# Performance work log

Hardware: AMD Instinct MI355X
Metric: run time of the kernel (lower is better)

The kernel has to match this reference:

```python
import jax, jax.numpy as jnp
import numpy as np

EMBED_DIM = 1024
NUM_HEADS = 16
HEAD_DIM = EMBED_DIM // NUM_HEADS
B, N = 4, 2048
EPS = 1e-5


def rotate_half(x):
    x2d = x.reshape(x.shape[:-1] + (-1, 2))
    x1, x2 = x2d[..., 0], x2d[..., 1]
    return jnp.stack([-x2, x1], axis=-1).reshape(x.shape)


def apply_rotary_emb(freqs, t):
    return t * freqs[0] + rotate_half(t) * freqs[1]


def setup_inputs() -> dict:
    key = jax.random.key(0)
    ks = jax.random.split(key, 12)
    d = EMBED_DIM
    inp = {
        "x": jax.random.normal(ks[0], (B, N, d), jnp.float32),
        "encoding": jax.random.normal(ks[1], (2, N, HEAD_DIM), jnp.float32),
        "Wqkv_w": jax.random.normal(ks[2], (d, 3 * d), jnp.float32) * (1.0 / np.sqrt(d)),
        "Wqkv_b": jnp.zeros((3 * d,), jnp.float32),
        "out_w": jax.random.normal(ks[3], (d, d), jnp.float32) * (1.0 / np.sqrt(d)),
        "out_b": jnp.zeros((d,), jnp.float32),
        "ffn0_w": jax.random.normal(ks[4], (2 * d, 2 * d), jnp.float32) * (1.0 / np.sqrt(2 * d)),
        "ffn0_b": jnp.zeros((2 * d,), jnp.float32),
        "ln_scale": jnp.ones((2 * d,), jnp.float32),
        "ln_bias": jnp.zeros((2 * d,), jnp.float32),
        "ffn3_w": jax.random.normal(ks[5], (2 * d, d), jnp.float32) * (1.0 / np.sqrt(2 * d)),
        "ffn3_b": jnp.zeros((d,), jnp.float32),
    }
    return inp


def reference(x, encoding, Wqkv_w, Wqkv_b, out_w, out_b, ffn0_w, ffn0_b, ln_scale, ln_bias, ffn3_w, ffn3_b):
    b, n, d = x.shape
    # fused QKV projection
    qkv = jnp.einsum('bnd,de->bne', x, Wqkv_w) + Wqkv_b
    qkv = qkv.reshape(b, n, NUM_HEADS, HEAD_DIM, 3).transpose(0, 2, 1, 3, 4)  # (b,h,n,hd,3)
    q, k, v = qkv[..., 0], qkv[..., 1], qkv[..., 2]
    # RoPE (encoding broadcasts over batch/heads)
    q = apply_rotary_emb(encoding, q)
    k = apply_rotary_emb(encoding, k)
    # attention (no mask)
    scale = 1.0 / jnp.sqrt(jnp.asarray(HEAD_DIM, x.dtype))
    logits = jnp.einsum('bhqd,bhkd->bhqk', q, k) * scale
    attn = jax.nn.softmax(logits, axis=-1)
    context = jnp.einsum('bhqk,bhkd->bhqd', attn, v)
    message = context.transpose(0, 2, 1, 3).reshape(b, n, d)
    message = jnp.einsum('bnd,de->bne', message, out_w) + out_b
    # FFN: concat -> Dense -> LayerNorm -> GELU(exact) -> Dense
    h = jnp.concatenate([x, message], axis=-1)
    h = jnp.einsum('bnd,de->bne', h, ffn0_w) + ffn0_b
    mu = jnp.mean(h, axis=-1, keepdims=True)
    var = jnp.mean(jnp.square(h - mu), axis=-1, keepdims=True)
    h = (h - mu) * jax.lax.rsqrt(var + EPS) * ln_scale + ln_bias
    h = jax.nn.gelu(h, approximate=False)
    res = jnp.einsum('bnd,de->bne', h, ffn3_w) + ffn3_b
    return x + res
```

## Files before the change

kernel.cpp:

```cpp
#include <hip/hip_runtime.h>
#include <hip/hip_bf16.h>
#include <math.h>

typedef __bf16 bf16x8 __attribute__((ext_vector_type(8)));
typedef float f32x4 __attribute__((ext_vector_type(4)));

#define MFMA16(a, b, c) __builtin_amdgcn_mfma_f32_16x16x32_bf16((a), (b), (c), 0, 0, 0)

__device__ __forceinline__ void gload16(const void* g, void* l) {
  __builtin_amdgcn_global_load_lds((const __attribute__((address_space(1))) void*)g,
                                   (__attribute__((address_space(3))) void*)l, 16, 0, 0);
}

#define BARRIER asm volatile("s_barrier" ::: "memory")

__device__ __forceinline__ void tr_body(float (*tile)[33], const float* __restrict__ in,
                                        int ldin, __bf16* __restrict__ out, int ldo,
                                        int n0, int k0, int t) {
  int tx = t & 31, ty = t >> 5;
#pragma unroll
  for (int r = 0; r < 32; r += 8)
    tile[ty + r][tx] = in[(size_t)(k0 + ty + r) * ldin + n0 + tx];
  __syncthreads();
#pragma unroll
  for (int r = 0; r < 32; r += 8)
    out[(size_t)(n0 + ty + r) * ldo + k0 + tx] = (__bf16)tile[tx][ty + r];
}

__global__ __launch_bounds__(256) void prep1(
    const float* __restrict__ wqkv, __bf16* __restrict__ wT_qkv,
    const float* __restrict__ wffn0, __bf16* __restrict__ wT_ffn0,
    __bf16* __restrict__ w0bT,
    const float* __restrict__ wffn3, __bf16* __restrict__ wT_ffn3,
    const float* __restrict__ wout, __bf16* __restrict__ wout_bf,
    const float* __restrict__ bqkv, float* __restrict__ bqkv_p,
    const float* __restrict__ bout, float* __restrict__ bias_part,
    const float* __restrict__ x, __bf16* __restrict__ h_in) {
  __shared__ float tile[32][33];
  const int bid = blockIdx.x;
  const int t = threadIdx.x;

  if (bid < 3072) {
    int bx = bid % 96, by = bid / 96;
    int n0 = bx * 32, k0 = by * 32;
    int tx = t & 31, ty = t >> 5;
#pragma unroll
    for (int r = 0; r < 32; r += 8)
      tile[ty + r][tx] = wqkv[(size_t)(k0 + ty + r) * 3072 + n0 + tx];
    __syncthreads();
#pragma unroll
    for (int r = 0; r < 32; r += 8) {
      int n = n0 + ty + r;
      int h = n / 192, rem = n % 192, hd = rem / 3, which = rem % 3;
      int np = which * 1024 + h * 64 + hd;
      wT_qkv[(size_t)np * 1024 + k0 + tx] = (__bf16)tile[tx][ty + r];
    }
  } else if (bid < 5120) {
    int lb = bid - 3072, bx = lb % 64, by = lb / 64;
    tr_body(tile, wffn0, 2048, wT_ffn0, 2048, bx * 32, by * 32, t);
  } else if (bid < 7168) {
    int lb = bid - 5120, bx = lb % 64, by = lb / 64;
    tr_body(tile, wffn0 + (size_t)1024 * 2048, 2048, w0bT, 1024, bx * 32, by * 32, t);
  } else if (bid < 9216) {
    int lb = bid - 7168, bx = lb % 32, by = lb / 32;
    tr_body(tile, wffn3, 1024, wT_ffn3, 2048, bx * 32, by * 32, t);
  } else if (bid < 9728) {
    int id = (bid - 9216) * 256 + t;
    const float* src = wout + (size_t)id * 8;
    __bf16 tmp[8];
#pragma unroll
    for (int e = 0; e < 8; ++e) tmp[e] = (__bf16)src[e];
    *(uint4*)(wout_bf + (size_t)id * 8) = *(uint4*)tmp;
  } else if (bid < 9740) {
    int n = (bid - 9728) * 256 + t;
    if (n < 3072) {
      int h = n / 192, rem = n % 192, hd = rem / 3, which = rem % 3;
      bqkv_p[which * 1024 + h * 64 + hd] = bqkv[n];
    }
  } else if (bid < 9868) {
    int lb = bid - 9740;
    int n = (lb % 8) * 256 + t;
    int e0 = (lb / 8) * 64;
    float s = 0.f;
#pragma unroll 4
    for (int e = 0; e < 64; ++e)
      s += bout[e0 + e] * wffn0[(size_t)(1024 + e0 + e) * 2048 + n];
    bias_part[(size_t)(lb / 8) * 2048 + n] = s;
  } else {
    int id = (bid - 9868) * 256 + t;
    int row = id >> 7, cc = id & 127;
    const float* src = x + (size_t)row * 1024 + cc * 8;
    __bf16 tmp[8];
#pragma unroll
    for (int e = 0; e < 8; ++e) tmp[e] = (__bf16)src[e];
    *(uint4*)(h_in + (size_t)row * 2048 + cc * 8) = *(uint4*)tmp;
  }
}

__global__ __launch_bounds__(256) void prep2(
    const __bf16* __restrict__ w0bT, const __bf16* __restrict__ wout_bf,
    __bf16* __restrict__ wT_ffn0,
    const float* __restrict__ bias_part, const float* __restrict__ bffn0,
    float* __restrict__ bffn0_f) {
  const int bid = blockIdx.x;
  const int t = threadIdx.x;
  if (bid >= 128) {
    int n = (bid - 128) * 256 + t;
    float s = bffn0[n];
#pragma unroll
    for (int y = 0; y < 16; ++y) s += bias_part[(size_t)y * 2048 + n];
    bffn0_f[n] = s;
    return;
  }
  __shared__ __attribute__((aligned(16))) __bf16 As[128 * 64];
  __shared__ __attribute__((aligned(16))) __bf16 Bs[128 * 64];
  const int row0A = (bid % 16) * 128;
  const int row0B = (bid / 16) * 128;
  const int wave = t >> 6, lane = t & 63;
  const int wm = wave >> 1, wn = wave & 1;
  const int g = lane >> 4, lr = lane & 15;
  f32x4 acc[4][4] = {};
  for (int k0 = 0; k0 < 1024; k0 += 64) {
#pragma unroll
    for (int p = 0; p < 4; ++p) {
      int cbase = (wave * 4 + p) * 64;
      int ci = cbase + lane;
      int r = ci >> 3, cp = ci & 7, cl = cp ^ (r & 7);
      gload16(w0bT + (size_t)(row0A + r) * 1024 + k0 + cl * 8, &As[cbase * 8]);
      gload16(wout_bf + (size_t)(row0B + r) * 1024 + k0 + cl * 8, &Bs[cbase * 8]);
    }
    __syncthreads();
#pragma unroll
    for (int kk = 0; kk < 2; ++kk) {
      bf16x8 af[4], bfr[4];
#pragma unroll
      for (int mt = 0; mt < 4; ++mt) {
        int r = wm * 64 + mt * 16 + lr, c = kk * 4 + g;
        af[mt] = *(const bf16x8*)((char*)As + r * 128 + ((c ^ (r & 7)) * 16));
      }
#pragma unroll
      for (int nt = 0; nt < 4; ++nt) {
        int r = wn * 64 + nt * 16 + lr, c = kk * 4 + g;
        bfr[nt] = *(const bf16x8*)((char*)Bs + r * 128 + ((c ^ (r & 7)) * 16));
      }
#pragma unroll
      for (int mt = 0; mt < 4; ++mt)
#pragma unroll
        for (int nt = 0; nt < 4; ++nt)
          acc[mt][nt] = MFMA16(af[mt], bfr[nt], acc[mt][nt]);
    }
    __syncthreads();
  }
#pragma unroll
  for (int mt = 0; mt < 4; ++mt) {
    int grow_base = row0A + wm * 64 + mt * 16 + g * 4;
#pragma unroll
    for (int nt = 0; nt < 4; ++nt) {
      int gcol = row0B + wn * 64 + nt * 16 + lr;
#pragma unroll
      for (int j = 0; j < 4; ++j)
        wT_ffn0[(size_t)(grow_base + j) * 2048 + 1024 + gcol] = (__bf16)acc[mt][nt][j];
    }
  }
}

template <typename OutT, bool HAS_RES, bool HAS_BIAS>
__global__ __launch_bounds__(256) void gemm_kernel(
    const __bf16* __restrict__ A, int lda,
    const __bf16* __restrict__ Bt,
    const float* __restrict__ bias,
    OutT* __restrict__ C, int ldc,
    const float* __restrict__ res,
    int M, int Nn, int K) {
  __shared__ __attribute__((aligned(16))) __bf16 As[128 * 64];
  __shared__ __attribute__((aligned(16))) __bf16 Bs[128 * 64];

  const int t = threadIdx.x;
  const int row0A = blockIdx.x * 128;
  const int row0B = blockIdx.y * 128;
  const int wave = t >> 6, lane = t & 63;
  const int wm = wave >> 1, wn = wave & 1;
  const int g = lane >> 4, lr = lane & 15;

  f32x4 acc[4][4] = {};

  for (int k0 = 0; k0 < K; k0 += 64) {
#pragma unroll
    for (int p = 0; p < 4; ++p) {
      int cbase = (wave * 4 + p) * 64;
      int ci = cbase + lane;
      int r = ci >> 3, cp = ci & 7, cl = cp ^ (r & 7);
      gload16(A + (size_t)(row0A + r) * lda + k0 + cl * 8, &As[cbase * 8]);
      gload16(Bt + (size_t)(row0B + r) * K + k0 + cl * 8, &Bs[cbase * 8]);
    }
    __syncthreads();
#pragma unroll
    for (int kk = 0; kk < 2; ++kk) {
      bf16x8 af[4], bfr[4];
#pragma unroll
      for (int mt = 0; mt < 4; ++mt) {
        int r = wm * 64 + mt * 16 + lr, c = kk * 4 + g;
        af[mt] = *(const bf16x8*)((char*)As + r * 128 + ((c ^ (r & 7)) * 16));
      }
#pragma unroll
      for (int nt = 0; nt < 4; ++nt) {
        int r = wn * 64 + nt * 16 + lr, c = kk * 4 + g;
        bfr[nt] = *(const bf16x8*)((char*)Bs + r * 128 + ((c ^ (r & 7)) * 16));
      }
#pragma unroll
      for (int mt = 0; mt < 4; ++mt)
#pragma unroll
        for (int nt = 0; nt < 4; ++nt)
          acc[mt][nt] = MFMA16(af[mt], bfr[nt], acc[mt][nt]);
    }
    __syncthreads();
  }

  float bias_v[4];
#pragma unroll
  for (int nt = 0; nt < 4; ++nt)
    bias_v[nt] = HAS_BIAS ? bias[row0B + wn * 64 + nt * 16 + lr] : 0.f;
#pragma unroll
  for (int mt = 0; mt < 4; ++mt) {
    int grow_base = row0A + wm * 64 + mt * 16 + g * 4;
#pragma unroll
    for (int nt = 0; nt < 4; ++nt) {
      int gcol = row0B + wn * 64 + nt * 16 + lr;
#pragma unroll
      for (int j = 0; j < 4; ++j) {
        int grow = grow_base + j;
        float v = acc[mt][nt][j] + bias_v[nt];
        if (HAS_RES) v += res[(size_t)grow * ldc + gcol];
        C[(size_t)grow * ldc + gcol] = (OutT)v;
      }
    }
  }
}

template <typename OutT>
__global__ __launch_bounds__(512, 2) void gemm256p(
    const __bf16* __restrict__ A, int lda,
    const __bf16* __restrict__ Bt, int ldb,
    const float* __restrict__ bias,
    OutT* __restrict__ C, int ldc, int K) {
  __shared__ __attribute__((aligned(16))) __bf16 As[2][256 * 64];
  __shared__ __attribute__((aligned(16))) __bf16 Bs[2][256 * 64];

  const int t = threadIdx.x;
  const int wave = t >> 6, lane = t & 63;
  const int wm = wave >> 2, wn = wave & 3;
  const int g = lane >> 4, lr = lane & 15;
  const int row0A = blockIdx.x * 256, row0B = blockIdx.y * 256;
  const int L = K >> 6;

  f32x4 acc[8][4] = {};

#define STG_A(tile, i)                                                        \
  {                                                                           \
    int cb = ((i) * 8 + wave) * 64;                                           \
    int ci = cb + lane;                                                       \
    int r = ci >> 3, cl = (ci & 7) ^ (r & 7);                                 \
    gload16(A + (size_t)(row0A + r) * lda + (size_t)(tile) * 64 + cl * 8,     \
            &As[(tile) & 1][cb * 8]);                                         \
  }
#define STG_B(tile, i)                                                        \
  {                                                                           \
    int cb = ((i) * 8 + wave) * 64;                                           \
    int ci = cb + lane;                                                       \
    int r = ci >> 3, cl = (ci & 7) ^ (r & 7);                                 \
    gload16(Bt + (size_t)(row0B + r) * ldb + (size_t)(tile) * 64 + cl * 8,    \
            &Bs[(tile) & 1][cb * 8]);                                         \
  }
#define AFRAG(d, mi, ks)                                                      \
  (*(const bf16x8*)((const char*)As[d] + (wm * 128 + (mi) * 16 + lr) * 128 +  \
                    ((((ks) * 4 + g) ^ (lr & 7)) * 16)))
#define BFRAG(d, ni, ks)                                                      \
  (*(const bf16x8*)((const char*)Bs[d] + (wn * 64 + (ni) * 16 + lr) * 128 +   \
                    ((((ks) * 4 + g) ^ (lr & 7)) * 16)))

#pragma unroll
  for (int i = 0; i < 4; ++i) STG_A(0, i);
#pragma unroll
  for (int i = 0; i < 4; ++i) STG_B(0, i);
  STG_A(1, 0);
  STG_A(1, 1);
  asm volatile("s_waitcnt vmcnt(2)" ::: "memory");
  BARRIER;

  for (int tt = 0; tt < L; ++tt) {
    const int d = tt & 1;
    const bool s1 = (tt + 1) < L, s2 = (tt + 2) < L;
    bf16x8 aL[4][2], aH[4][2], bL[2][2], bH[2][2];

#pragma unroll
    for (int mi = 0; mi < 4; ++mi) {
      aL[mi][0] = AFRAG(d, mi, 0);
      aL[mi][1] = AFRAG(d, mi, 1);
    }
#pragma unroll
    for (int ni = 0; ni < 2; ++ni) {
      bL[ni][0] = BFRAG(d, ni, 0);
      bL[ni][1] = BFRAG(d, ni, 1);
    }
    if (s1) { STG_A(tt + 1, 2); STG_A(tt + 1, 3); }
    BARRIER;
    __builtin_amdgcn_s_setprio(1);
#pragma unroll
    for (int mi = 0; mi < 4; ++mi)
#pragma unroll
      for (int ni = 0; ni < 2; ++ni) {
        acc[mi][ni] = MFMA16(aL[mi][0], bL[ni][0], acc[mi][ni]);
        acc[mi][ni] = MFMA16(aL[mi][1], bL[ni][1], acc[mi][ni]);
      }
    __builtin_amdgcn_s_setprio(0);
    BARRIER;

#pragma unroll
    for (int ni = 0; ni < 2; ++ni) {
      bH[ni][0] = BFRAG(d, ni + 2, 0);
      bH[ni][1] = BFRAG(d, ni + 2, 1);
    }
    if (s1) { STG_B(tt + 1, 0); STG_B(tt + 1, 1); }
    BARRIER;
    __builtin_amdgcn_s_setprio(1);
#pragma unroll
    for (int mi = 0; mi < 4; ++mi)
#pragma unroll
      for (int ni = 0; ni < 2; ++ni) {
        acc[mi][ni + 2] = MFMA16(aL[mi][0], bH[ni][0], acc[mi][ni + 2]);
        acc[mi][ni + 2] = MFMA16(aL[mi][1], bH[ni][1], acc[mi][ni + 2]);
      }
    __builtin_amdgcn_s_setprio(0);
    BARRIER;

#pragma unroll
    for (int mi = 0; mi < 4; ++mi) {
      aH[mi][0] = AFRAG(d, mi + 4, 0);
      aH[mi][1] = AFRAG(d, mi + 4, 1);
    }
    if (s1) { STG_B(tt + 1, 2); STG_B(tt + 1, 3); }
    BARRIER;
    __builtin_amdgcn_s_setprio(1);
#pragma unroll
    for (int mi = 0; mi < 4; ++mi)
#pragma unroll
      for (int ni = 0; ni < 2; ++ni) {
        acc[mi + 4][ni + 2] = MFMA16(aH[mi][0], bH[ni][0], acc[mi + 4][ni + 2]);
        acc[mi + 4][ni + 2] = MFMA16(aH[mi][1], bH[ni][1], acc[mi + 4][ni + 2]);
      }
    __builtin_amdgcn_s_setprio(0);
    BARRIER;

    if (s2) { STG_A(tt + 2, 0); STG_A(tt + 2, 1); }
    __builtin_amdgcn_s_setprio(1);
#pragma unroll
    for (int mi = 0; mi < 4; ++mi)
#pragma unroll
      for (int ni = 0; ni < 2; ++ni) {
        acc[mi + 4][ni] = MFMA16(aH[mi][0], bL[ni][0], acc[mi + 4][ni]);
        acc[mi + 4][ni] = MFMA16(aH[mi][1], bL[ni][1], acc[mi + 4][ni]);
      }
    __builtin_amdgcn_s_setprio(0);
    if (s2)
      asm volatile("s_waitcnt vmcnt(2)" ::: "memory");
    else
      asm volatile("s_waitcnt vmcnt(0)" ::: "memory");
    BARRIER;
  }
#undef STG_A
#undef STG_B
#undef AFRAG
#undef BFRAG

  float bias_v[4];
#pragma unroll
  for (int ni = 0; ni < 4; ++ni) bias_v[ni] = bias[row0B + wn * 64 + ni * 16 + lr];
#pragma unroll
  for (int mi = 0; mi < 8; ++mi) {
    int grow_base = row0A + wm * 128 + mi * 16 + g * 4;
#pragma unroll
    for (int ni = 0; ni < 4; ++ni) {
      int gcol = row0B + wn * 64 + ni * 16 + lr;
#pragma unroll
      for (int j = 0; j < 4; ++j)
        C[(size_t)(grow_base + j) * ldc + gcol] = (OutT)(acc[mi][ni][j] + bias_v[ni]);
    }
  }
}

__global__ __launch_bounds__(256) void rope_scatter(
    const __bf16* __restrict__ qkv, const float* __restrict__ enc,
    __bf16* __restrict__ q, __bf16* __restrict__ kk, __bf16* __restrict__ vt) {
  int bh = blockIdx.y;
  int b = bh >> 4, h = bh & 15;
  int n0 = blockIdx.x * 64;
  int t = threadIdx.x;
  const float QSC = 0.125f * 1.44269504088896f;
#pragma unroll
  for (int i = 0; i < 2; ++i) {
    int id = t + i * 256;
    int nl = id >> 3, cc = id & 7;
    int n = n0 + nl;
    size_t row = (size_t)(b * 2048 + n) * 3072;
    bf16x8 qv = *(const bf16x8*)(qkv + row + h * 64 + cc * 8);
    bf16x8 kv = *(const bf16x8*)(qkv + row + 1024 + h * 64 + cc * 8);
    const float* e0 = enc + (size_t)n * 64 + cc * 8;
    const float* e1 = e0 + 131072;
    __bf16 qo[8], ko[8];
#pragma unroll
    for (int e = 0; e < 8; e += 2) {
      float q0 = (float)qv[e], q1 = (float)qv[e + 1];
      float k0 = (float)kv[e], k1 = (float)kv[e + 1];
      float f00 = e0[e], f01 = e0[e + 1], f10 = e1[e], f11 = e1[e + 1];
      qo[e] = (__bf16)((q0 * f00 - q1 * f10) * QSC);
      qo[e + 1] = (__bf16)((q1 * f01 + q0 * f11) * QSC);
      ko[e] = (__bf16)(k0 * f00 - k1 * f10);
      ko[e + 1] = (__bf16)(k1 * f01 + k0 * f11);
    }
    size_t qb = ((size_t)bh * 2048 + n) * 64 + cc * 8;
    *(uint4*)(q + qb) = *(uint4*)qo;
    *(uint4*)(kk + qb) = *(uint4*)ko;
  }
#pragma unroll
  for (int i = 0; i < 2; ++i) {
    int id = t + i * 256;
    int hd = id >> 3, c = id & 7;
    __bf16 tmp[8];
#pragma unroll
    for (int e = 0; e < 8; ++e) {
      int kv = (c >> 2) * 32 + (e >> 2) * 16 + (c & 3) * 4 + (e & 3);
      int n = n0 + kv;
      tmp[e] = qkv[(size_t)(b * 2048 + n) * 3072 + 2048 + h * 64 + hd];
    }
    *(uint4*)(vt + ((size_t)bh * 64 + hd) * 2048 + n0 + c * 8) = *(uint4*)tmp;
  }
}

__global__ __launch_bounds__(256) void attn_kernel(
    const __bf16* __restrict__ q, const __bf16* __restrict__ k,
    const __bf16* __restrict__ vt, __bf16* __restrict__ ctx) {
  __shared__ __attribute__((aligned(16))) __bf16 Ks[2][64 * 64];
  __shared__ __attribute__((aligned(16))) __bf16 Vs[2][64 * 64];

  int bid0 = blockIdx.y * gridDim.x + blockIdx.x;
  int bid = (bid0 & 7) * 64 + (bid0 >> 3);
  const int bh = bid >> 3, qblk = bid & 7;
  const int b = bh >> 4, h = bh & 15;
  const int q0 = qblk * 256;
  const int t = threadIdx.x, wave = t >> 6, lane = t & 63;
  const int g = lane >> 4, lr = lane & 15;
  const int qrow0 = q0 + wave * 64;

  const __bf16* kbase = k + (size_t)bh * 2048 * 64;
  const __bf16* vbase = vt + (size_t)bh * 64 * 2048;

  bf16x8 qf[4][2];
#pragma unroll
  for (int u = 0; u < 4; ++u)
#pragma unroll
    for (int kc = 0; kc < 2; ++kc)
      qf[u][kc] = *(const bf16x8*)(q + ((size_t)bh * 2048 + qrow0 + u * 16 + lr) * 64 +
                                   kc * 32 + g * 8);

  bf16x8 ones;
#pragma unroll
  for (int e = 0; e < 8; ++e) ones[e] = (__bf16)1.0f;

  f32x4 o[4][4] = {};
  f32x4 lacc[4] = {};

#define STAGE_ATTN(buf, kv0)                                                    \
  {                                                                             \
    _Pragma("unroll") for (int p = 0; p < 2; ++p) {                             \
      int cbase = wave * 128 + p * 64;                                          \
      int ci = cbase + lane;                                                    \
      int r = ci >> 3, cp = ci & 7, cl = cp ^ (r & 7);                          \
      gload16(kbase + (size_t)((kv0) + r) * 64 + cl * 8, &Ks[buf][cbase * 8]);  \
      gload16(vbase + (size_t)r * 2048 + (kv0) + cl * 8, &Vs[buf][cbase * 8]);  \
    }                                                                           \
  }

  STAGE_ATTN(0, 0);
  __syncthreads();
  int buf = 0;

  for (int kv0 = 0; kv0 < 2048; kv0 += 64) {
    if (kv0 + 64 < 2048) STAGE_ATTN(buf ^ 1, kv0 + 64);

    bf16x8 kf[4][2];
#pragma unroll
    for (int nt = 0; nt < 4; ++nt) {
      int r = nt * 16 + lr;
      kf[nt][0] = *(const bf16x8*)((char*)Ks[buf] + r * 128 + ((g ^ (r & 7)) * 16));
      kf[nt][1] = *(const bf16x8*)((char*)Ks[buf] + r * 128 + (((4 + g) ^ (r & 7)) * 16));
    }

    bf16x8 pf[4][2];
#pragma unroll
    for (int u = 0; u < 4; ++u) {
      f32x4 s[4];
      __builtin_amdgcn_s_setprio(1);
#pragma unroll
      for (int nt = 0; nt < 4; ++nt) {
        f32x4 a = {};
        a = MFMA16(kf[nt][0], qf[u][0], a);
        a = MFMA16(kf[nt][1], qf[u][1], a);
        s[nt] = a;
      }
      __builtin_amdgcn_s_setprio(0);
#pragma unroll
      for (int t2 = 0; t2 < 2; ++t2)
#pragma unroll
        for (int e = 0; e < 8; ++e)
          pf[u][t2][e] = (__bf16)__builtin_amdgcn_exp2f(s[2 * t2 + (e >> 2)][e & 3]);
    }

    __builtin_amdgcn_s_setprio(1);
#pragma unroll
    for (int u = 0; u < 4; ++u) {
      lacc[u] = MFMA16(ones, pf[u][0], lacc[u]);
      lacc[u] = MFMA16(ones, pf[u][1], lacc[u]);
    }
#pragma unroll
    for (int t2 = 0; t2 < 2; ++t2)
#pragma unroll
      for (int nt = 0; nt < 4; ++nt) {
        int r = nt * 16 + lr;
        bf16x8 vf = *(const bf16x8*)((char*)Vs[buf] + r * 128 + (((t2 * 4 + g) ^ (r & 7)) * 16));
#pragma unroll
        for (int u = 0; u < 4; ++u) o[u][nt] = MFMA16(vf, pf[u][t2], o[u][nt]);
      }
    __builtin_amdgcn_s_setprio(0);
    __syncthreads();
    buf ^= 1;
  }

#pragma unroll
  for (int u = 0; u < 4; ++u) {
    float inv = 1.f / lacc[u][0];
    size_t obase = ((size_t)(b * 2048 + qrow0 + u * 16 + lr)) * 2048 + 1024 + h * 64;
#pragma unroll
    for (int nt = 0; nt < 4; ++nt) {
      __bf16 w4[4];
#pragma unroll
      for (int j = 0; j < 4; ++j) w4[j] = (__bf16)(o[u][nt][j] * inv);
      *(uint2*)(ctx + obase + nt * 16 + g * 4) = *(uint2*)w4;
    }
  }
#undef STAGE_ATTN
}

__global__ __launch_bounds__(256) void ln_gelu(const __bf16* __restrict__ hin,
                                               const float* __restrict__ lns,
                                               const float* __restrict__ lnb,
                                               __bf16* __restrict__ hout) {
  int row = blockIdx.x;
  const __bf16* rp = hin + (size_t)row * 2048;
  int t = threadIdx.x;
  __bf16 tmp[8];
  *(uint4*)tmp = *(const uint4*)(rp + t * 8);
  float vals[8], s = 0.f, s2 = 0.f;
#pragma unroll
  for (int e = 0; e < 8; ++e) {
    float x = (float)tmp[e];
    vals[e] = x;
    s += x;
    s2 += x * x;
  }
#pragma unroll
  for (int m = 1; m < 64; m <<= 1) {
    s += __shfl_xor(s, m, 64);
    s2 += __shfl_xor(s2, m, 64);
  }
  __shared__ float red[8];
  int wave = t >> 6, lane = t & 63;
  if (lane == 0) { red[wave] = s; red[4 + wave] = s2; }
  __syncthreads();
  s = red[0] + red[1] + red[2] + red[3];
  s2 = red[4] + red[5] + red[6] + red[7];
  float mu = s * (1.f / 2048.f);
  float var = s2 * (1.f / 2048.f) - mu * mu;
  float rstd = rsqrtf(var + 1e-5f);
  __bf16 outv[8];
#pragma unroll
  for (int e = 0; e < 8; ++e) {
    int c = t * 8 + e;
    float xh = (vals[e] - mu) * rstd * lns[c] + lnb[c];
    float gg = 0.5f * xh * (1.f + erff(xh * 0.70710678118f));
    outv[e] = (__bf16)gg;
  }
  *(uint4*)(hout + (size_t)row * 2048 + t * 8) = *(uint4*)outv;
}

extern "C" void kernel_launch(void* const* d_in, const int* in_sizes, int n_in,
                              void* d_out, int out_size, void* d_ws, size_t ws_size,
                              hipStream_t stream) {
  const float* x = (const float*)d_in[0];
  const float* enc = (const float*)d_in[1];
  const float* wqkv = (const float*)d_in[2];
  const float* bqkv = (const float*)d_in[3];
  const float* wout = (const float*)d_in[4];
  const float* bout = (const float*)d_in[5];
  const float* wffn0 = (const float*)d_in[6];
  const float* bffn0 = (const float*)d_in[7];
  const float* lns = (const float*)d_in[8];
  const float* lnb = (const float*)d_in[9];
  const float* wffn3 = (const float*)d_in[10];
  const float* bffn3 = (const float*)d_in[11];
  float* out = (float*)d_out;
  char* ws = (char*)d_ws;

  __bf16* wT_qkv = (__bf16*)(ws + 0);
  __bf16* wT_ffn0 = (__bf16*)(ws + 6291456);
  __bf16* wT_ffn3 = (__bf16*)(ws + 14680064);
  __bf16* wout_bf = (__bf16*)(ws + 18874368);
  __bf16* w0bT = (__bf16*)(ws + 20971520);
  float* bias_part = (float*)(ws + 25165824);
  float* bqkv_p = (float*)(ws + 25296896);
  float* bffn0_f = (float*)(ws + 25309184);
  __bf16* h_in = (__bf16*)(ws + 25317376);
  __bf16* qkv = (__bf16*)(ws + 58871808);
  __bf16* ffn0o = qkv;
  __bf16* qb = (__bf16*)(ws + 109203456);
  __bf16* h2 = qb;
  __bf16* kb = (__bf16*)(ws + 125980672);
  __bf16* vtb = (__bf16*)(ws + 142757888);

  dim3 blk(256);
  prep1<<<13964, blk, 0, stream>>>(wqkv, wT_qkv, wffn0, wT_ffn0, w0bT, wffn3, wT_ffn3,
                                   wout, wout_bf, bqkv, bqkv_p, bout, bias_part, x, h_in);
  prep2<<<136, blk, 0, stream>>>(w0bT, wout_bf, wT_ffn0, bias_part, bffn0, bffn0_f);

  gemm256p<__bf16><<<dim3(32, 12), dim3(512), 0, stream>>>(
      h_in, 2048, wT_qkv, 1024, bqkv_p, qkv, 3072, 1024);

  rope_scatter<<<dim3(32, 64), blk, 0, stream>>>(qkv, enc, qb, kb, vtb);
  attn_kernel<<<dim3(8, 64), blk, 0, stream>>>(qb, kb, vtb, h_in);

  gemm256p<__bf16><<<dim3(32, 8), dim3(512), 0, stream>>>(
      h_in, 2048, wT_ffn0, 2048, bffn0_f, ffn0o, 2048, 2048);

  ln_gelu<<<8192, blk, 0, stream>>>(ffn0o, lns, lnb, h2);

  gemm_kernel<float, true, true><<<dim3(64, 8), blk, 0, stream>>>(
      h2, 2048, wT_ffn3, bffn3, out, 1024, x, 8192, 1024, 2048);
}
```

Measured before the change: 372.5 us.

## Fuse RoPE and Q/K/V scatter into QKV GEMM epilogue; halve attention query tile

The QKV GEMM epilogue now applies RoPE and scaling and writes Q, K and transposed V straight into their per-head layouts. This removes the separate rope_scatter kernel and the round trip of the full qkv intermediate through memory. A transposed copy of the encoding table is made in prep1 so the epilogue can read it with float4 loads, and V is transposed through LDS. Separately, attention now handles 128 query rows per block instead of 256, doubling the grid for better occupancy and cutting register pressure, at the cost of reloading K/V tiles more often.

```diff
diff --git a/kernel.cpp b/kernel.cpp
--- a/kernel.cpp
+++ b/kernel.cpp
@@ -35,7 +35,8 @@
     const float* __restrict__ wout, __bf16* __restrict__ wout_bf,
     const float* __restrict__ bqkv, float* __restrict__ bqkv_p,
     const float* __restrict__ bout, float* __restrict__ bias_part,
-    const float* __restrict__ x, __bf16* __restrict__ h_in) {
+    const float* __restrict__ x, __bf16* __restrict__ h_in,
+    const float* __restrict__ enc, float* __restrict__ encT) {
   __shared__ float tile[32][33];
   const int bid = blockIdx.x;
   const int t = threadIdx.x;
@@ -86,7 +87,7 @@
     for (int e = 0; e < 64; ++e)
       s += bout[e0 + e] * wffn0[(size_t)(1024 + e0 + e) * 2048 + n];
     bias_part[(size_t)(lb / 8) * 2048 + n] = s;
-  } else {
+  } else if (bid < 13964) {
     int id = (bid - 9868) * 256 + t;
     int row = id >> 7, cc = id & 127;
     const float* src = x + (size_t)row * 1024 + cc * 8;
@@ -94,6 +95,19 @@
 #pragma unroll
     for (int e = 0; e < 8; ++e) tmp[e] = (__bf16)src[e];
     *(uint4*)(h_in + (size_t)row * 2048 + cc * 8) = *(uint4*)tmp;
+  } else {
+    int lb = bid - 13964;
+    int tab = lb >> 7, lb2 = lb & 127;
+    int n0 = (lb2 & 1) * 32;
+    int k0 = (lb2 >> 1) * 32;
+    int tx = t & 31, ty = t >> 5;
+#pragma unroll
+    for (int r = 0; r < 32; r += 8)
+      tile[ty + r][tx] = enc[(size_t)tab * 131072 + (size_t)(k0 + ty + r) * 64 + n0 + tx];
+    __syncthreads();
+#pragma unroll
+    for (int r = 0; r < 32; r += 8)
+      encT[(size_t)tab * 131072 + (size_t)(n0 + ty + r) * 2048 + k0 + tx] = tile[tx][ty + r];
   }
 }
 
@@ -237,12 +251,14 @@
   }
 }
 
-template <typename OutT>
+template <typename OutT, int MODE>
 __global__ __launch_bounds__(512, 2) void gemm256p(
     const __bf16* __restrict__ A, int lda,
     const __bf16* __restrict__ Bt, int ldb,
     const float* __restrict__ bias,
-    OutT* __restrict__ C, int ldc, int K) {
+    OutT* __restrict__ C, int ldc, int K,
+    __bf16* __restrict__ qb, __bf16* __restrict__ kb,
+    __bf16* __restrict__ vtb, const float* __restrict__ encT) {
   __shared__ __attribute__((aligned(16))) __bf16 As[2][256 * 64];
   __shared__ __attribute__((aligned(16))) __bf16 Bs[2][256 * 64];
 
@@ -375,64 +391,78 @@
   float bias_v[4];
 #pragma unroll
   for (int ni = 0; ni < 4; ++ni) bias_v[ni] = bias[row0B + wn * 64 + ni * 16 + lr];
-#pragma unroll
-  for (int mi = 0; mi < 8; ++mi) {
-    int grow_base = row0A + wm * 128 + mi * 16 + g * 4;
-#pragma unroll
-    for (int ni = 0; ni < 4; ++ni) {
-      int gcol = row0B + wn * 64 + ni * 16 + lr;
-#pragma unroll
-      for (int j = 0; j < 4; ++j)
-        C[(size_t)(grow_base + j) * ldc + gcol] = (OutT)(acc[mi][ni][j] + bias_v[ni]);
-    }
-  }
-}
-
-__global__ __launch_bounds__(256) void rope_scatter(
-    const __bf16* __restrict__ qkv, const float* __restrict__ enc,
-    __bf16* __restrict__ q, __bf16* __restrict__ kk, __bf16* __restrict__ vt) {
-  int bh = blockIdx.y;
-  int b = bh >> 4, h = bh & 15;
-  int n0 = blockIdx.x * 64;
-  int t = threadIdx.x;
-  const float QSC = 0.125f * 1.44269504088896f;
-#pragma unroll
-  for (int i = 0; i < 2; ++i) {
-    int id = t + i * 256;
-    int nl = id >> 3, cc = id & 7;
-    int n = n0 + nl;
-    size_t row = (size_t)(b * 2048 + n) * 3072;
-    bf16x8 qv = *(const bf16x8*)(qkv + row + h * 64 + cc * 8);
-    bf16x8 kv = *(const bf16x8*)(qkv + row + 1024 + h * 64 + cc * 8);
-    const float* e0 = enc + (size_t)n * 64 + cc * 8;
-    const float* e1 = e0 + 131072;
-    __bf16 qo[8], ko[8];
-#pragma unroll
-    for (int e = 0; e < 8; e += 2) {
-      float q0 = (float)qv[e], q1 = (float)qv[e + 1];
-      float k0 = (float)kv[e], k1 = (float)kv[e + 1];
-      float f00 = e0[e], f01 = e0[e + 1], f10 = e1[e], f11 = e1[e + 1];
-      qo[e] = (__bf16)((q0 * f00 - q1 * f10) * QSC);
-      qo[e + 1] = (__bf16)((q1 * f01 + q0 * f11) * QSC);
-      ko[e] = (__bf16)(k0 * f00 - k1 * f10);
-      ko[e + 1] = (__bf16)(k1 * f01 + k0 * f11);
-    }
-    size_t qb = ((size_t)bh * 2048 + n) * 64 + cc * 8;
-    *(uint4*)(q + qb) = *(uint4*)qo;
-    *(uint4*)(kk + qb) = *(uint4*)ko;
-  }
-#pragma unroll
-  for (int i = 0; i < 2; ++i) {
-    int id = t + i * 256;
-    int hd = id >> 3, c = id & 7;
-    __bf16 tmp[8];
-#pragma unroll
-    for (int e = 0; e < 8; ++e) {
-      int kv = (c >> 2) * 32 + (e >> 2) * 16 + (c & 3) * 4 + (e & 3);
-      int n = n0 + kv;
-      tmp[e] = qkv[(size_t)(b * 2048 + n) * 3072 + 2048 + h * 64 + hd];
-    }
-    *(uint4*)(vt + ((size_t)bh * 64 + hd) * 2048 + n0 + c * 8) = *(uint4*)tmp;
+
+  if (MODE == 0) {
+#pragma unroll
+    for (int mi = 0; mi < 8; ++mi) {
+      int grow_base = row0A + wm * 128 + mi * 16 + g * 4;
+#pragma unroll
+      for (int ni = 0; ni < 4; ++ni) {
+        int gcol = row0B + wn * 64 + ni * 16 + lr;
+#pragma unroll
+        for (int j = 0; j < 4; ++j)
+          C[(size_t)(grow_base + j) * ldc + gcol] = (OutT)(acc[mi][ni][j] + bias_v[ni]);
+      }
+    }
+  } else {
+    const int which = blockIdx.y >> 2;
+    const int h = (blockIdx.y & 3) * 4 + wn;
+    const int b = blockIdx.x >> 3;
+    const int bh = b * 16 + h;
+    const int ntop = (blockIdx.x & 7) * 256 + wm * 128;
+
+    if (which < 2) {
+      __bf16* dst = (which == 0) ? qb : kb;
+      const float sc = (which == 0) ? 0.125f * 1.44269504088896f : 1.f;
+      const float sgn = (lane & 1) ? 1.f : -1.f;
+#pragma unroll
+      for (int mi = 0; mi < 8; ++mi) {
+#pragma unroll
+        for (int ni = 0; ni < 4; ++ni) {
+          int hd = ni * 16 + lr;
+          const float* p0 = encT + (size_t)hd * 2048 + ntop + mi * 16 + g * 4;
+          float4 f0 = *(const float4*)p0;
+          float4 f1 = *(const float4*)(p0 + 131072);
+#pragma unroll
+          for (int j = 0; j < 4; ++j) {
+            float v = acc[mi][ni][j] + bias_v[ni];
+            float p = __shfl_xor(v, 1, 64);
+            float e0 = ((const float*)&f0)[j], e1 = ((const float*)&f1)[j];
+            float r = (v * e0 + sgn * p * e1) * sc;
+            dst[((size_t)bh * 2048 + ntop + mi * 16 + g * 4 + j) * 64 + hd] = (__bf16)r;
+          }
+        }
+      }
+    } else {
+      char* lbuf = (char*)As;
+      const int wb2 = wave * 16384;
+#pragma unroll
+      for (int mi = 0; mi < 8; ++mi)
+#pragma unroll
+        for (int ni = 0; ni < 4; ++ni) {
+          int hd = ni * 16 + lr;
+          int tok = mi * 16 + g * 4;
+          __bf16 w4[4];
+#pragma unroll
+          for (int j = 0; j < 4; ++j) w4[j] = (__bf16)(acc[mi][ni][j] + bias_v[ni]);
+          int ab = wb2 + hd * 256 + ((tok * 2) ^ ((hd & 15) << 4));
+          *(uint2*)(lbuf + ab) = *(uint2*)w4;
+        }
+      __syncthreads();
+#pragma unroll
+      for (int it = 0; it < 16; ++it) {
+        int hd = (lane >> 3) + (it & 7) * 8;
+        int slot = (lane & 7) + (it >> 3) * 8;
+        int grp = slot >> 3, c = slot & 7;
+        int kv0 = grp * 64 + (c >> 2) * 32 + (c & 3) * 4;
+        int a1 = wb2 + hd * 256 + ((kv0 * 2) ^ ((hd & 15) << 4));
+        int a2 = wb2 + hd * 256 + (((kv0 + 16) * 2) ^ ((hd & 15) << 4));
+        uint2 lo = *(uint2*)(lbuf + a1);
+        uint2 hi = *(uint2*)(lbuf + a2);
+        uint4 o4 = make_uint4(lo.x, lo.y, hi.x, hi.y);
+        *(uint4*)(vtb + ((size_t)bh * 64 + hd) * 2048 + ntop + grp * 64 + c * 8) = o4;
+      }
+    }
   }
 }
 
@@ -442,21 +472,22 @@
   __shared__ __attribute__((aligned(16))) __bf16 Ks[2][64 * 64];
   __shared__ __attribute__((aligned(16))) __bf16 Vs[2][64 * 64];
 
+  int nwg = gridDim.x * gridDim.y;
   int bid0 = blockIdx.y * gridDim.x + blockIdx.x;
-  int bid = (bid0 & 7) * 64 + (bid0 >> 3);
-  const int bh = bid >> 3, qblk = bid & 7;
+  int bid = (bid0 & 7) * (nwg >> 3) + (bid0 >> 3);
+  const int bh = bid >> 4, qblk = bid & 15;
   const int b = bh >> 4, h = bh & 15;
-  const int q0 = qblk * 256;
+  const int q0 = qblk * 128;
   const int t = threadIdx.x, wave = t >> 6, lane = t & 63;
   const int g = lane >> 4, lr = lane & 15;
-  const int qrow0 = q0 + wave * 64;
+  const int qrow0 = q0 + wave * 32;
 
   const __bf16* kbase = k + (size_t)bh * 2048 * 64;
   const __bf16* vbase = vt + (size_t)bh * 64 * 2048;
 
-  bf16x8 qf[4][2];
-#pragma unroll
-  for (int u = 0; u < 4; ++u)
+  bf16x8 qf[2][2];
+#pragma unroll
+  for (int u = 0; u < 2; ++u)
 #pragma unroll
     for (int kc = 0; kc < 2; ++kc)
       qf[u][kc] = *(const bf16x8*)(q + ((size_t)bh * 2048 + qrow0 + u * 16 + lr) * 64 +
@@ -466,8 +497,8 @@
 #pragma unroll
   for (int e = 0; e < 8; ++e) ones[e] = (__bf16)1.0f;
 
-  f32x4 o[4][4] = {};
-  f32x4 lacc[4] = {};
+  f32x4 o[2][4] = {};
+  f32x4 lacc[2] = {};
 
 #define STAGE_ATTN(buf, kv0)                                                    \
   {                                                                             \
@@ -487,56 +518,49 @@
   for (int kv0 = 0; kv0 < 2048; kv0 += 64) {
     if (kv0 + 64 < 2048) STAGE_ATTN(buf ^ 1, kv0 + 64);
 
-    bf16x8 kf[4][2];
+    f32x4 s[2][4];
+    __builtin_amdgcn_s_setprio(1);
 #pragma unroll
     for (int nt = 0; nt < 4; ++nt) {
       int r = nt * 16 + lr;
-      kf[nt][0] = *(const bf16x8*)((char*)Ks[buf] + r * 128 + ((g ^ (r & 7)) * 16));
-      kf[nt][1] = *(const bf16x8*)((char*)Ks[buf] + r * 128 + (((4 + g) ^ (r & 7)) * 16));
-    }
-
-    bf16x8 pf[4][2];
-#pragma unroll
-    for (int u = 0; u < 4; ++u) {
-      f32x4 s[4];
+      bf16x8 kf0 = *(const bf16x8*)((char*)Ks[buf] + r * 128 + ((g ^ (r & 7)) * 16));
+      bf16x8 kf1 = *(const bf16x8*)((char*)Ks[buf] + r * 128 + (((4 + g) ^ (r & 7)) * 16));
+#pragma unroll
+      for (int u = 0; u < 2; ++u) {
+        f32x4 a = {};
+        a = MFMA16(kf0, qf[u][0], a);
+        a = MFMA16(kf1, qf[u][1], a);
+        s[u][nt] = a;
+      }
+    }
+    __builtin_amdgcn_s_setprio(0);
+
+#pragma unroll
+    for (int t2 = 0; t2 < 2; ++t2) {
+      bf16x8 pf[2];
+#pragma unroll
+      for (int u = 0; u < 2; ++u) {
+#pragma unroll
+        for (int e = 0; e < 8; ++e)
+          pf[u][e] = (__bf16)__builtin_amdgcn_exp2f(s[u][2 * t2 + (e >> 2)][e & 3]);
+        lacc[u] = MFMA16(ones, pf[u], lacc[u]);
+      }
       __builtin_amdgcn_s_setprio(1);
-#pragma unroll
-      for (int nt = 0; nt < 4; ++nt) {
-        f32x4 a = {};
-        a = MFMA16(kf[nt][0], qf[u][0], a);
-        a = MFMA16(kf[nt][1], qf[u][1], a);
-        s[nt] = a;
-      }
-      __builtin_amdgcn_s_setprio(0);
-#pragma unroll
-      for (int t2 = 0; t2 < 2; ++t2)
-#pragma unroll
-        for (int e = 0; e < 8; ++e)
-          pf[u][t2][e] = (__bf16)__builtin_amdgcn_exp2f(s[2 * t2 + (e >> 2)][e & 3]);
-    }
-
-    __builtin_amdgcn_s_setprio(1);
-#pragma unroll
-    for (int u = 0; u < 4; ++u) {
-      lacc[u] = MFMA16(ones, pf[u][0], lacc[u]);
-      lacc[u] = MFMA16(ones, pf[u][1], lacc[u]);
-    }
-#pragma unroll
-    for (int t2 = 0; t2 < 2; ++t2)
 #pragma unroll
       for (int nt = 0; nt < 4; ++nt) {
         int r = nt * 16 + lr;
         bf16x8 vf = *(const bf16x8*)((char*)Vs[buf] + r * 128 + (((t2 * 4 + g) ^ (r & 7)) * 16));
 #pragma unroll
-        for (int u = 0; u < 4; ++u) o[u][nt] = MFMA16(vf, pf[u][t2], o[u][nt]);
-      }
-    __builtin_amdgcn_s_setprio(0);
+        for (int u = 0; u < 2; ++u) o[u][nt] = MFMA16(vf, pf[u], o[u][nt]);
+      }
+      __builtin_amdgcn_s_setprio(0);
+    }
     __syncthreads();
     buf ^= 1;
   }
 
 #pragma unroll
-  for (int u = 0; u < 4; ++u) {
+  for (int u = 0; u < 2; ++u) {
     float inv = 1.f / lacc[u][0];
     size_t obase = ((size_t)(b * 2048 + qrow0 + u * 16 + lr)) * 2048 + 1024 + h * 64;
 #pragma unroll
@@ -619,26 +643,27 @@
   float* bqkv_p = (float*)(ws + 25296896);
   float* bffn0_f = (float*)(ws + 25309184);
   __bf16* h_in = (__bf16*)(ws + 25317376);
-  __bf16* qkv = (__bf16*)(ws + 58871808);
-  __bf16* ffn0o = qkv;
+  __bf16* ffn0o = (__bf16*)(ws + 58871808);
   __bf16* qb = (__bf16*)(ws + 109203456);
   __bf16* h2 = qb;
   __bf16* kb = (__bf16*)(ws + 125980672);
   __bf16* vtb = (__bf16*)(ws + 142757888);
+  float* encT = (float*)(ws + 159535104);
 
   dim3 blk(256);
-  prep1<<<13964, blk, 0, stream>>>(wqkv, wT_qkv, wffn0, wT_ffn0, w0bT, wffn3, wT_ffn3,
-                                   wout, wout_bf, bqkv, bqkv_p, bout, bias_part, x, h_in);
+  prep1<<<14220, blk, 0, stream>>>(wqkv, wT_qkv, wffn0, wT_ffn0, w0bT, wffn3, wT_ffn3,
+                                   wout, wout_bf, bqkv, bqkv_p, bout, bias_part, x, h_in,
+                                   enc, encT);
   prep2<<<136, blk, 0, stream>>>(w0bT, wout_bf, wT_ffn0, bias_part, bffn0, bffn0_f);
 
-  gemm256p<__bf16><<<dim3(32, 12), dim3(512), 0, stream>>>(
-      h_in, 2048, wT_qkv, 1024, bqkv_p, qkv, 3072, 1024);
-
-  rope_scatter<<<dim3(32, 64), blk, 0, stream>>>(qkv, enc, qb, kb, vtb);
-  attn_kernel<<<dim3(8, 64), blk, 0, stream>>>(qb, kb, vtb, h_in);
-
-  gemm256p<__bf16><<<dim3(32, 8), dim3(512), 0, stream>>>(
-      h_in, 2048, wT_ffn0, 2048, bffn0_f, ffn0o, 2048, 2048);
+  gemm256p<__bf16, 1><<<dim3(32, 12), dim3(512), 0, stream>>>(
+      h_in, 2048, wT_qkv, 1024, bqkv_p, (__bf16*)nullptr, 0, 1024, qb, kb, vtb, encT);
+
+  attn_kernel<<<dim3(16, 64), blk, 0, stream>>>(qb, kb, vtb, h_in);
+
+  gemm256p<__bf16, 0><<<dim3(32, 8), dim3(512), 0, stream>>>(
+      h_in, 2048, wT_ffn0, 2048, bffn0_f, ffn0o, 2048, 2048,
+      nullptr, nullptr, nullptr, nullptr);
 
   ln_gelu<<<8192, blk, 0, stream>>>(ffn0o, lns, lnb, h2);
 
```

New measurement: 365.0 us. -2.0%, faster.

## Replace 256-tile GEMMs with generic GEMM and halve attention query tile

Applied to the files above, without the earlier changes.

Removes the 256x256 ping-pong GEMM kernel and routes the QKV and FFN0 projections through the existing 128-tile gemm_kernel with larger grids. The attention kernel now handles 128 query rows per block (32 per wave), doubling the grid to 1024 blocks. It also interleaves exp, row-sum and PV MFMAs per half-tile to cut register pressure. This trades per-tile data reuse for more parallelism and occupancy, but risks losing the efficiency of the tuned large-tile GEMM.

```diff
diff --git a/kernel.cpp b/kernel.cpp
--- a/kernel.cpp
+++ b/kernel.cpp
@@ -11,8 +11,6 @@
   __builtin_amdgcn_global_load_lds((const __attribute__((address_space(1))) void*)g,
                                    (__attribute__((address_space(3))) void*)l, 16, 0, 0);
 }
-
-#define BARRIER asm volatile("s_barrier" ::: "memory")
 
 __device__ __forceinline__ void tr_body(float (*tile)[33], const float* __restrict__ in,
                                         int ldin, __bf16* __restrict__ out, int ldo,
@@ -237,157 +235,6 @@
   }
 }
 
-template <typename OutT>
-__global__ __launch_bounds__(512, 2) void gemm256p(
-    const __bf16* __restrict__ A, int lda,
-    const __bf16* __restrict__ Bt, int ldb,
-    const float* __restrict__ bias,
-    OutT* __restrict__ C, int ldc, int K) {
-  __shared__ __attribute__((aligned(16))) __bf16 As[2][256 * 64];
-  __shared__ __attribute__((aligned(16))) __bf16 Bs[2][256 * 64];
-
-  const int t = threadIdx.x;
-  const int wave = t >> 6, lane = t & 63;
-  const int wm = wave >> 2, wn = wave & 3;
-  const int g = lane >> 4, lr = lane & 15;
-  const int row0A = blockIdx.x * 256, row0B = blockIdx.y * 256;
-  const int L = K >> 6;
-
-  f32x4 acc[8][4] = {};
-
-#define STG_A(tile, i)                                                        \
-  {                                                                           \
-    int cb = ((i) * 8 + wave) * 64;                                           \
-    int ci = cb + lane;                                                       \
-    int r = ci >> 3, cl = (ci & 7) ^ (r & 7);                                 \
-    gload16(A + (size_t)(row0A + r) * lda + (size_t)(tile) * 64 + cl * 8,     \
-            &As[(tile) & 1][cb * 8]);                                         \
-  }
-#define STG_B(tile, i)                                                        \
-  {                                                                           \
-    int cb = ((i) * 8 + wave) * 64;                                           \
-    int ci = cb + lane;                                                       \
-    int r = ci >> 3, cl = (ci & 7) ^ (r & 7);                                 \
-    gload16(Bt + (size_t)(row0B + r) * ldb + (size_t)(tile) * 64 + cl * 8,    \
-            &Bs[(tile) & 1][cb * 8]);                                         \
-  }
-#define AFRAG(d, mi, ks)                                                      \
-  (*(const bf16x8*)((const char*)As[d] + (wm * 128 + (mi) * 16 + lr) * 128 +  \
-                    ((((ks) * 4 + g) ^ (lr & 7)) * 16)))
-#define BFRAG(d, ni, ks)                                                      \
-  (*(const bf16x8*)((const char*)Bs[d] + (wn * 64 + (ni) * 16 + lr) * 128 +   \
-                    ((((ks) * 4 + g) ^ (lr & 7)) * 16)))
-
-#pragma unroll
-  for (int i = 0; i < 4; ++i) STG_A(0, i);
-#pragma unroll
-  for (int i = 0; i < 4; ++i) STG_B(0, i);
-  STG_A(1, 0);
-  STG_A(1, 1);
-  asm volatile("s_waitcnt vmcnt(2)" ::: "memory");
-  BARRIER;
-
-  for (int tt = 0; tt < L; ++tt) {
-    const int d = tt & 1;
-    const bool s1 = (tt + 1) < L, s2 = (tt + 2) < L;
-    bf16x8 aL[4][2], aH[4][2], bL[2][2], bH[2][2];
-
-#pragma unroll
-    for (int mi = 0; mi < 4; ++mi) {
-      aL[mi][0] = AFRAG(d, mi, 0);
-      aL[mi][1] = AFRAG(d, mi, 1);
-    }
-#pragma unroll
-    for (int ni = 0; ni < 2; ++ni) {
-      bL[ni][0] = BFRAG(d, ni, 0);
-      bL[ni][1] = BFRAG(d, ni, 1);
-    }
-    if (s1) { STG_A(tt + 1, 2); STG_A(tt + 1, 3); }
-    BARRIER;
-    __builtin_amdgcn_s_setprio(1);
-#pragma unroll
-    for (int mi = 0; mi < 4; ++mi)
-#pragma unroll
-      for (int ni = 0; ni < 2; ++ni) {
-        acc[mi][ni] = MFMA16(aL[mi][0], bL[ni][0], acc[mi][ni]);
-        acc[mi][ni] = MFMA16(aL[mi][1], bL[ni][1], acc[mi][ni]);
-      }
-    __builtin_amdgcn_s_setprio(0);
-    BARRIER;
-
-#pragma unroll
-    for (int ni = 0; ni < 2; ++ni) {
-      bH[ni][0] = BFRAG(d, ni + 2, 0);
-      bH[ni][1] = BFRAG(d, ni + 2, 1);
-    }
-    if (s1) { STG_B(tt + 1, 0); STG_B(tt + 1, 1); }
-    BARRIER;
-    __builtin_amdgcn_s_setprio(1);
-#pragma unroll
-    for (int mi = 0; mi < 4; ++mi)
-#pragma unroll
-      for (int ni = 0; ni < 2; ++ni) {
-        acc[mi][ni + 2] = MFMA16(aL[mi][0], bH[ni][0], acc[mi][ni + 2]);
-        acc[mi][ni + 2] = MFMA16(aL[mi][1], bH[ni][1], acc[mi][ni + 2]);
-      }
-    __builtin_amdgcn_s_setprio(0);
-    BARRIER;
-
-#pragma unroll
-    for (int mi = 0; mi < 4; ++mi) {
-      aH[mi][0] = AFRAG(d, mi + 4, 0);
-      aH[mi][1] = AFRAG(d, mi + 4, 1);
-    }
-    if (s1) { STG_B(tt + 1, 2); STG_B(tt + 1, 3); }
-    BARRIER;
-    __builtin_amdgcn_s_setprio(1);
-#pragma unroll
-    for (int mi = 0; mi < 4; ++mi)
-#pragma unroll
-      for (int ni = 0; ni < 2; ++ni) {
-        acc[mi + 4][ni + 2] = MFMA16(aH[mi][0], bH[ni][0], acc[mi + 4][ni + 2]);
-        acc[mi + 4][ni + 2] = MFMA16(aH[mi][1], bH[ni][1], acc[mi + 4][ni + 2]);
-      }
-    __builtin_amdgcn_s_setprio(0);
-    BARRIER;
-
-    if (s2) { STG_A(tt + 2, 0); STG_A(tt + 2, 1); }
-    __builtin_amdgcn_s_setprio(1);
-#pragma unroll
-    for (int mi = 0; mi < 4; ++mi)
-#pragma unroll
-      for (int ni = 0; ni < 2; ++ni) {
-        acc[mi + 4][ni] = MFMA16(aH[mi][0], bL[ni][0], acc[mi + 4][ni]);
-        acc[mi + 4][ni] = MFMA16(aH[mi][1], bL[ni][1], acc[mi + 4][ni]);
-      }
-    __builtin_amdgcn_s_setprio(0);
-    if (s2)
-      asm volatile("s_waitcnt vmcnt(2)" ::: "memory");
-    else
-      asm volatile("s_waitcnt vmcnt(0)" ::: "memory");
-    BARRIER;
-  }
-#undef STG_A
-#undef STG_B
-#undef AFRAG
-#undef BFRAG
-
-  float bias_v[4];
-#pragma unroll
-  for (int ni = 0; ni < 4; ++ni) bias_v[ni] = bias[row0B + wn * 64 + ni * 16 + lr];
-#pragma unroll
-  for (int mi = 0; mi < 8; ++mi) {
-    int grow_base = row0A + wm * 128 + mi * 16 + g * 4;
-#pragma unroll
-    for (int ni = 0; ni < 4; ++ni) {
-      int gcol = row0B + wn * 64 + ni * 16 + lr;
-#pragma unroll
-      for (int j = 0; j < 4; ++j)
-        C[(size_t)(grow_base + j) * ldc + gcol] = (OutT)(acc[mi][ni][j] + bias_v[ni]);
-    }
-  }
-}
-
 __global__ __launch_bounds__(256) void rope_scatter(
     const __bf16* __restrict__ qkv, const float* __restrict__ enc,
     __bf16* __restrict__ q, __bf16* __restrict__ kk, __bf16* __restrict__ vt) {
@@ -442,21 +289,22 @@
   __shared__ __attribute__((aligned(16))) __bf16 Ks[2][64 * 64];
   __shared__ __attribute__((aligned(16))) __bf16 Vs[2][64 * 64];
 
+  int nwg = gridDim.x * gridDim.y;
   int bid0 = blockIdx.y * gridDim.x + blockIdx.x;
-  int bid = (bid0 & 7) * 64 + (bid0 >> 3);
-  const int bh = bid >> 3, qblk = bid & 7;
+  int bid = (bid0 & 7) * (nwg >> 3) + (bid0 >> 3);
+  const int bh = bid >> 4, qblk = bid & 15;
   const int b = bh >> 4, h = bh & 15;
-  const int q0 = qblk * 256;
+  const int q0 = qblk * 128;
   const int t = threadIdx.x, wave = t >> 6, lane = t & 63;
   const int g = lane >> 4, lr = lane & 15;
-  const int qrow0 = q0 + wave * 64;
+  const int qrow0 = q0 + wave * 32;
 
   const __bf16* kbase = k + (size_t)bh * 2048 * 64;
   const __bf16* vbase = vt + (size_t)bh * 64 * 2048;
 
-  bf16x8 qf[4][2];
-#pragma unroll
-  for (int u = 0; u < 4; ++u)
+  bf16x8 qf[2][2];
+#pragma unroll
+  for (int u = 0; u < 2; ++u)
 #pragma unroll
     for (int kc = 0; kc < 2; ++kc)
       qf[u][kc] = *(const bf16x8*)(q + ((size_t)bh * 2048 + qrow0 + u * 16 + lr) * 64 +
@@ -466,8 +314,8 @@
 #pragma unroll
   for (int e = 0; e < 8; ++e) ones[e] = (__bf16)1.0f;
 
-  f32x4 o[4][4] = {};
-  f32x4 lacc[4] = {};
+  f32x4 o[2][4] = {};
+  f32x4 lacc[2] = {};
 
 #define STAGE_ATTN(buf, kv0)                                                    \
   {                                                                             \
@@ -487,56 +335,49 @@
   for (int kv0 = 0; kv0 < 2048; kv0 += 64) {
     if (kv0 + 64 < 2048) STAGE_ATTN(buf ^ 1, kv0 + 64);
 
-    bf16x8 kf[4][2];
+    f32x4 s[2][4];
+    __builtin_amdgcn_s_setprio(1);
 #pragma unroll
     for (int nt = 0; nt < 4; ++nt) {
       int r = nt * 16 + lr;
-      kf[nt][0] = *(const bf16x8*)((char*)Ks[buf] + r * 128 + ((g ^ (r & 7)) * 16));
-      kf[nt][1] = *(const bf16x8*)((char*)Ks[buf] + r * 128 + (((4 + g) ^ (r & 7)) * 16));
-    }
-
-    bf16x8 pf[4][2];
-#pragma unroll
-    for (int u = 0; u < 4; ++u) {
-      f32x4 s[4];
+      bf16x8 kf0 = *(const bf16x8*)((char*)Ks[buf] + r * 128 + ((g ^ (r & 7)) * 16));
+      bf16x8 kf1 = *(const bf16x8*)((char*)Ks[buf] + r * 128 + (((4 + g) ^ (r & 7)) * 16));
+#pragma unroll
+      for (int u = 0; u < 2; ++u) {
+        f32x4 a = {};
+        a = MFMA16(kf0, qf[u][0], a);
+        a = MFMA16(kf1, qf[u][1], a);
+        s[u][nt] = a;
+      }
+    }
+    __builtin_amdgcn_s_setprio(0);
+
+#pragma unroll
+    for (int t2 = 0; t2 < 2; ++t2) {
+      bf16x8 pf[2];
+#pragma unroll
+      for (int u = 0; u < 2; ++u) {
+#pragma unroll
+        for (int e = 0; e < 8; ++e)
+          pf[u][e] = (__bf16)__builtin_amdgcn_exp2f(s[u][2 * t2 + (e >> 2)][e & 3]);
+        lacc[u] = MFMA16(ones, pf[u], lacc[u]);
+      }
       __builtin_amdgcn_s_setprio(1);
-#pragma unroll
-      for (int nt = 0; nt < 4; ++nt) {
-        f32x4 a = {};
-        a = MFMA16(kf[nt][0], qf[u][0], a);
-        a = MFMA16(kf[nt][1], qf[u][1], a);
-        s[nt] = a;
-      }
-      __builtin_amdgcn_s_setprio(0);
-#pragma unroll
-      for (int t2 = 0; t2 < 2; ++t2)
-#pragma unroll
-        for (int e = 0; e < 8; ++e)
-          pf[u][t2][e] = (__bf16)__builtin_amdgcn_exp2f(s[2 * t2 + (e >> 2)][e & 3]);
-    }
-
-    __builtin_amdgcn_s_setprio(1);
-#pragma unroll
-    for (int u = 0; u < 4; ++u) {
-      lacc[u] = MFMA16(ones, pf[u][0], lacc[u]);
-      lacc[u] = MFMA16(ones, pf[u][1], lacc[u]);
-    }
-#pragma unroll
-    for (int t2 = 0; t2 < 2; ++t2)
 #pragma unroll
       for (int nt = 0; nt < 4; ++nt) {
         int r = nt * 16 + lr;
         bf16x8 vf = *(const bf16x8*)((char*)Vs[buf] + r * 128 + (((t2 * 4 + g) ^ (r & 7)) * 16));
 #pragma unroll
-        for (int u = 0; u < 4; ++u) o[u][nt] = MFMA16(vf, pf[u][t2], o[u][nt]);
-      }
-    __builtin_amdgcn_s_setprio(0);
+        for (int u = 0; u < 2; ++u) o[u][nt] = MFMA16(vf, pf[u], o[u][nt]);
+      }
+      __builtin_amdgcn_s_setprio(0);
+    }
     __syncthreads();
     buf ^= 1;
   }
 
 #pragma unroll
-  for (int u = 0; u < 4; ++u) {
+  for (int u = 0; u < 2; ++u) {
     float inv = 1.f / lacc[u][0];
     size_t obase = ((size_t)(b * 2048 + qrow0 + u * 16 + lr)) * 2048 + 1024 + h * 64;
 #pragma unroll
@@ -631,14 +472,14 @@
                                    wout, wout_bf, bqkv, bqkv_p, bout, bias_part, x, h_in);
   prep2<<<136, blk, 0, stream>>>(w0bT, wout_bf, wT_ffn0, bias_part, bffn0, bffn0_f);
 
-  gemm256p<__bf16><<<dim3(32, 12), dim3(512), 0, stream>>>(
-      h_in, 2048, wT_qkv, 1024, bqkv_p, qkv, 3072, 1024);
+  gemm_kernel<__bf16, false, true><<<dim3(64, 24), blk, 0, stream>>>(
+      h_in, 2048, wT_qkv, bqkv_p, qkv, 3072, nullptr, 8192, 3072, 1024);
 
   rope_scatter<<<dim3(32, 64), blk, 0, stream>>>(qkv, enc, qb, kb, vtb);
-  attn_kernel<<<dim3(8, 64), blk, 0, stream>>>(qb, kb, vtb, h_in);
-
-  gemm256p<__bf16><<<dim3(32, 8), dim3(512), 0, stream>>>(
-      h_in, 2048, wT_ffn0, 2048, bffn0_f, ffn0o, 2048, 2048);
+  attn_kernel<<<dim3(16, 64), blk, 0, stream>>>(qb, kb, vtb, h_in);
+
+  gemm_kernel<__bf16, false, true><<<dim3(64, 16), blk, 0, stream>>>(
+      h_in, 2048, wT_ffn0, bffn0_f, ffn0o, 2048, nullptr, 8192, 2048, 2048);
 
   ln_gelu<<<8192, blk, 0, stream>>>(ffn0o, lns, lnb, h2);
 
```

Result: slower. 388.6 us (+4.3%).
